# Performance work log

Measured on AMD Instinct MI355X. Metric: run time of the kernel, lower is better.

## Reference

```python
import jax, jax.numpy as jnp
import numpy as np

FSIZE = 128   # fsize
ANUM = 16     # number of agents
CNUM = 2048   # number of cities
BATCH = 64


def setup_inputs() -> dict:
    key = jax.random.key(0)
    ks = jax.random.split(key, 6)
    f = FSIZE
    N = CNUM + 2 * ANUM
    s = 0.02
    return {
        "nfeature": jax.random.normal(ks[0], (BATCH, f, N), jnp.float32),
        # torch Linear weights are [out, in]
        "Wg": jax.random.normal(ks[1], (f, 4 * f), jnp.float32) * s,   # glb_embedding
        "bg": jnp.zeros((f,), jnp.float32),
        "Wc": jax.random.normal(ks[2], (3 * f, 2 * f), jnp.float32) * s,  # city_embedding
        "bc": jnp.zeros((3 * f,), jnp.float32),
        "Wa": jax.random.normal(ks[3], (f, 3 * f), jnp.float32) * s,   # agent_embedding
        "ba": jnp.zeros((f,), jnp.float32),
        "Wp": jax.random.normal(ks[4], (f, f), jnp.float32) * s,       # project_out
        "bp": jnp.zeros((f,), jnp.float32),
        "step": 1,
        "anum": ANUM,
    }


def reference(nfeature, Wg, bg, Wc, bc, Wa, ba, Wp, bp, step, anum):
    nf = jnp.transpose(nfeature, (0, 2, 1))  # [B, N, f]
    B, N, f = nf.shape
    cnum = N - 2 * anum
    city = nf[:, :cnum]                       # [B, cnum, f]
    a_start = nf[:, cnum:cnum + anum]         # [B, anum, f]
    a_end = nf[:, cnum + anum:]               # [B, anum, f]

    # global context via max pooling over segments -> glb_embedding
    glb = jnp.concatenate([nf.max(1), city.max(1), a_start.max(1), a_end.max(1)], axis=1)  # [B, 4f]
    deglb = (glb @ Wg.T + bg)[:, None, :]     # [B, 1, f]

    # mean-pooled global context -> same glb_embedding -> free agent token
    ave = jnp.concatenate([nf.mean(1), city.mean(1), a_start.mean(1), a_end.mean(1)], axis=1)
    free_agent = (ave @ Wg.T + bg)[:, None, :]  # [B, 1, f]

    # city keys/values/logit-keys: x, y, z
    city_feat = jnp.concatenate([jnp.broadcast_to(deglb, (B, cnum, f)), city], axis=2)  # [B, cnum, 2f]
    xyz = city_feat @ Wc.T + bc               # [B, cnum, 3f]
    x, y, z = jnp.split(xyz, 3, axis=2)       # each [B, cnum, f]

    # agent queries
    agent_feat = jnp.concatenate(
        [jnp.broadcast_to(deglb, (B, anum, f)), a_start, a_end], axis=2)  # [B, anum, 3f]
    af = agent_feat @ Wa.T + ba               # [B, anum, f]
    if step > 0:
        af = jnp.concatenate([af, free_agent], axis=1)  # [B, anum+1, f]

    scale = 1.0 / jnp.sqrt(jnp.float32(f))
    ucj = jnp.einsum('baf,bcf->bac', af, x) * scale           # [B, A, cnum]
    new_af = jnp.einsum('bac,bcf->baf', jax.nn.softmax(ucj, axis=2), y)
    new_af = new_af @ Wp.T + bp                                # project_out
    logits = jnp.tanh(jnp.einsum('baf,bcf->bac', new_af, z) * scale) * 10.0  # [B, A, cnum]
    probs = jax.nn.softmax(jnp.transpose(logits, (0, 2, 1)), axis=2)         # [B, cnum, A]
    return probs
```

## Files before the change

kernel.cpp:

```cpp
#include <hip/hip_runtime.h>
#include <math.h>

#define F 128
#define NTOT 2080
#define CN 2048
#define AN 16
#define NA 17
#define CHK 128
#define NCHK 16

__device__ __forceinline__ float wmax(float v){
  #pragma unroll
  for(int m=32;m;m>>=1) v = fmaxf(v, __shfl_xor(v, m, 64));
  return v;
}
__device__ __forceinline__ float wsum(float v){
  #pragma unroll
  for(int m=32;m;m>>=1) v += __shfl_xor(v, m, 64);
  return v;
}

__global__ __launch_bounds__(256) void k0t_transpose(
      const float* __restrict__ Wg, const float* __restrict__ Wc,
      const float* __restrict__ Wp, const float* __restrict__ Wa,
      float* __restrict__ WgT, float* __restrict__ WcT,
      float* __restrict__ WpT, float* __restrict__ WaT){
  __shared__ float tile[32][33];
  const int z = blockIdx.z;
  const float* src; float* dst; int R, C;
  if(z==0){ src=Wg; dst=WgT; R=128; C=512; }
  else if(z==1){ src=Wc; dst=WcT; R=384; C=256; }
  else if(z==2){ src=Wp; dst=WpT; R=128; C=128; }
  else { src=Wa; dst=WaT; R=128; C=384; }
  const int c0 = blockIdx.x*32, r0 = blockIdx.y*32;
  if(c0>=C || r0>=R) return;
  const int tx = threadIdx.x&31, ty = threadIdx.x>>5;
  #pragma unroll
  for(int rr=0;rr<4;rr++)
    tile[ty+rr*8][tx] = src[(size_t)(r0+ty+rr*8)*C + c0 + tx];
  __syncthreads();
  #pragma unroll
  for(int rr=0;rr<4;rr++)
    dst[(size_t)(c0+ty+rr*8)*R + r0 + tx] = tile[tx][ty+rr*8];
}

__global__ __launch_bounds__(128) void k0a_wpy(const float* __restrict__ Wp, const float* __restrict__ Wc,
                                               float* __restrict__ Wpy){
  const int k = blockIdx.x, i = threadIdx.x;
  float acc = 0.f;
  const float* wp = Wp + (size_t)k*F;
  for(int j=0;j<F;j++) acc += wp[j]*Wc[(size_t)(128+j)*256 + 128 + i];
  Wpy[k*F+i] = acc;
}

__global__ __launch_bounds__(128) void k0b_m1(const float* __restrict__ Wc, const float* __restrict__ Wpy,
                                              float* __restrict__ M1){
  const int jc = blockIdx.x, i = threadIdx.x;
  float acc = 0.f;
  for(int k=0;k<F;k++) acc += Wc[(size_t)(256+k)*256 + 128 + jc]*Wpy[k*F+i];
  M1[jc*F+i] = acc;
}

__global__ __launch_bounds__(256) void k1_reduce(const float* __restrict__ nf,
                                                 float* __restrict__ glb, float* __restrict__ ave){
  const int jg = blockIdx.x, b = blockIdx.y;
  const int w = threadIdx.x>>6, lane = threadIdx.x&63;
  const int j = jg*4 + w;
  const float4* row = (const float4*)(nf + (size_t)(b*F + j)*NTOT);
  float cmax=-INFINITY, csum=0.f, smax=-INFINITY, ssum=0.f, emax=-INFINITY, esum=0.f;
  for(int n4 = lane; n4 < 520; n4 += 64){
    float4 v = row[n4];
    float mx = fmaxf(fmaxf(v.x,v.y), fmaxf(v.z,v.w));
    float sm = (v.x+v.y)+(v.z+v.w);
    if(n4 < 512){ cmax=fmaxf(cmax,mx); csum+=sm; }
    else if(n4 < 516){ smax=fmaxf(smax,mx); ssum+=sm; }
    else { emax=fmaxf(emax,mx); esum+=sm; }
  }
  cmax=wmax(cmax); csum=wsum(csum); smax=wmax(smax); ssum=wsum(ssum); emax=wmax(emax); esum=wsum(esum);
  if(lane==0){
    const int gb = b*4*F;
    glb[gb + j]       = fmaxf(cmax, fmaxf(smax,emax));
    glb[gb + F + j]   = cmax;
    glb[gb + 2*F + j] = smax;
    glb[gb + 3*F + j] = emax;
    float tS = csum+ssum+esum;
    ave[gb + j]       = tS / 2080.f;
    ave[gb + F + j]   = csum / 2048.f;
    ave[gb + 2*F + j] = ssum / 16.f;
    ave[gb + 3*F + j] = esum / 16.f;
  }
}

__global__ __launch_bounds__(256) void k2a_prep(
    const float* __restrict__ WgT, const float* __restrict__ bg,
    const float* __restrict__ WcT, const float* __restrict__ Wc, const float* __restrict__ bc,
    const float* __restrict__ WpT, const float* __restrict__ bp,
    const float* __restrict__ Wpy,
    const float* __restrict__ glb, const float* __restrict__ ave,
    float* __restrict__ deglb_g, float* __restrict__ fa_g, float* __restrict__ cx,
    float* __restrict__ czc, float* __restrict__ vz, float* __restrict__ szc){
  const int b = blockIdx.x, tid = threadIdx.x;
  __shared__ float glb_s[512], ave_s[512];
  __shared__ float deglb_s[F], cvec_s[3*F], cpy_s[F];
  for(int i=tid;i<512;i+=256){ glb_s[i]=glb[b*512+i]; ave_s[i]=ave[b*512+i]; }
  __syncthreads();
  {
    const int j = tid&127;
    const float* src = (tid<128)? glb_s : ave_s;
    float a0=0.f,a1=0.f,a2=0.f,a3=0.f;
    for(int k=0;k<512;k+=4){
      a0 += WgT[(size_t)(k+0)*128+j]*src[k+0];
      a1 += WgT[(size_t)(k+1)*128+j]*src[k+1];
      a2 += WgT[(size_t)(k+2)*128+j]*src[k+2];
      a3 += WgT[(size_t)(k+3)*128+j]*src[k+3];
    }
    float d = (a0+a1)+(a2+a3) + bg[j];
    if(tid<128){ deglb_s[j]=d; deglb_g[b*F+j]=d; }
    else fa_g[b*F+j]=d;
  }
  __syncthreads();
  for(int i=tid;i<3*F;i+=256){
    float a0=0.f,a1=0.f,a2=0.f,a3=0.f;
    for(int k=0;k<F;k+=4){
      a0 += WcT[(size_t)(k+0)*384+i]*deglb_s[k+0];
      a1 += WcT[(size_t)(k+1)*384+i]*deglb_s[k+1];
      a2 += WcT[(size_t)(k+2)*384+i]*deglb_s[k+2];
      a3 += WcT[(size_t)(k+3)*384+i]*deglb_s[k+3];
    }
    float v = (a0+a1)+(a2+a3) + bc[i];
    cvec_s[i]=v;
    if(i<F) cx[b*F+i]=v;
  }
  __syncthreads();
  if(tid<128){
    const int j = tid;
    float a0=0.f,a1=0.f,a2=0.f,a3=0.f;
    for(int k=0;k<F;k+=4){
      a0 += WpT[(size_t)(k+0)*128+j]*cvec_s[128+k+0];
      a1 += WpT[(size_t)(k+1)*128+j]*cvec_s[128+k+1];
      a2 += WpT[(size_t)(k+2)*128+j]*cvec_s[128+k+2];
      a3 += WpT[(size_t)(k+3)*128+j]*cvec_s[128+k+3];
    }
    cpy_s[j] = (a0+a1)+(a2+a3) + bp[j];
  } else {
    const int j = tid-128;
    float a0=0.f,a1=0.f,a2=0.f,a3=0.f;
    for(int k=0;k<F;k+=4){
      a0 += Wpy[(size_t)(k+0)*128+j]*cvec_s[256+k+0];
      a1 += Wpy[(size_t)(k+1)*128+j]*cvec_s[256+k+1];
      a2 += Wpy[(size_t)(k+2)*128+j]*cvec_s[256+k+2];
      a3 += Wpy[(size_t)(k+3)*128+j]*cvec_s[256+k+3];
    }
    vz[b*F+j] = (a0+a1)+(a2+a3);
  }
  __syncthreads();
  if(tid<128){
    const int j = tid;
    float a0=0.f,a1=0.f,a2=0.f,a3=0.f;
    for(int k=0;k<F;k+=4){
      a0 += Wc[(size_t)(256+k+0)*256 + 128 + j]*cpy_s[k+0];
      a1 += Wc[(size_t)(256+k+1)*256 + 128 + j]*cpy_s[k+1];
      a2 += Wc[(size_t)(256+k+2)*256 + 128 + j]*cpy_s[k+2];
      a3 += Wc[(size_t)(256+k+3)*256 + 128 + j]*cpy_s[k+3];
    }
    czc[b*F+j] = (a0+a1)+(a2+a3);
  } else if(tid<192){
    const int lane = tid-128;
    float p = cpy_s[lane]*cvec_s[256+lane] + cpy_s[64+lane]*cvec_s[256+64+lane];
    p = wsum(p);
    if(lane==0) szc[b]=p;
  }
}

__global__ __launch_bounds__(256) void k2c_agents(
    const float* __restrict__ nf, const float* __restrict__ WaT, const float* __restrict__ ba,
    const float* __restrict__ Wc,
    const float* __restrict__ deglb_g, const float* __restrict__ fa_g, const float* __restrict__ cx,
    float* __restrict__ afx, float* __restrict__ sx){
  const int a = blockIdx.x, b = blockIdx.y, tid = threadIdx.x;
  __shared__ float src_s[384];
  __shared__ float af_s[F], cx_s[F];
  if(tid<128){ src_s[tid] = deglb_g[b*F+tid]; cx_s[tid]=cx[b*F+tid]; }
  else if(a<16){
    const int j = tid-128;
    src_s[128+j] = nf[(size_t)(b*F+j)*NTOT + CN + a];
    src_s[256+j] = nf[(size_t)(b*F+j)*NTOT + CN + AN + a];
  }
  __syncthreads();
  if(a<16){
    if(tid<128){
      const int j = tid;
      float a0=0.f,a1=0.f,a2=0.f,a3=0.f;
      for(int k=0;k<384;k+=4){
        a0 += WaT[(size_t)(k+0)*128+j]*src_s[k+0];
        a1 += WaT[(size_t)(k+1)*128+j]*src_s[k+1];
        a2 += WaT[(size_t)(k+2)*128+j]*src_s[k+2];
        a3 += WaT[(size_t)(k+3)*128+j]*src_s[k+3];
      }
      af_s[j] = (a0+a1)+(a2+a3) + ba[j];
    }
  } else if(tid<128){
    af_s[tid] = fa_g[b*F+tid];
  }
  __syncthreads();
  if(tid<128){
    const int j = tid;
    float a0=0.f,a1=0.f,a2=0.f,a3=0.f;
    for(int i=0;i<F;i+=4){
      a0 += af_s[i+0]*Wc[(size_t)(i+0)*256 + 128 + j];
      a1 += af_s[i+1]*Wc[(size_t)(i+1)*256 + 128 + j];
      a2 += af_s[i+2]*Wc[(size_t)(i+2)*256 + 128 + j];
      a3 += af_s[i+3]*Wc[(size_t)(i+3)*256 + 128 + j];
    }
    afx[((size_t)b*NA+a)*F + j] = (a0+a1)+(a2+a3);
  } else if(tid<192){
    const int lane = tid-128;
    float p = af_s[lane]*cx_s[lane] + af_s[64+lane]*cx_s[64+lane];
    p = wsum(p);
    if(lane==0) sx[b*NA+a]=p;
  }
}

__global__ __launch_bounds__(256) void k35_flash(const float* __restrict__ nf,
      const float* __restrict__ afx, const float* __restrict__ sx,
      float* __restrict__ pmax, float* __restrict__ psum, float* __restrict__ tpart){
  const int b = blockIdx.y, tid = threadIdx.x;
  const int chunk = blockIdx.x, c0 = chunk*CHK;
  __shared__ float afx_s[NA*F];
  __shared__ float sx_s[NA];
  __shared__ float at_s[NA*CHK];
  __shared__ float4 nf4_s[F*8];
  __shared__ float red_s[4][NA], red2_s[4][NA];
  for(int o=tid;o<NA*F;o+=256) afx_s[o]=afx[(size_t)b*NA*F+o];
  if(tid<NA) sx_s[tid]=sx[b*NA+tid];
  __syncthreads();
  const int kq = tid>>6;
  const int ct = tid&63;
  const int lane = tid&63, w = tid>>6;
  float2 acc[NA];
  #pragma unroll
  for(int a=0;a<NA;a++){ acc[a].x=0.f; acc[a].y=0.f; }
  {
    const float* base = nf + (size_t)b*F*NTOT + (size_t)(kq*32)*NTOT + c0 + 2*ct;
    #pragma unroll 2
    for(int q=0;q<8;q++){
      float2 l0 = *(const float2*)(base + (size_t)(q*4+0)*NTOT);
      float2 l1 = *(const float2*)(base + (size_t)(q*4+1)*NTOT);
      float2 l2 = *(const float2*)(base + (size_t)(q*4+2)*NTOT);
      float2 l3 = *(const float2*)(base + (size_t)(q*4+3)*NTOT);
      #pragma unroll
      for(int a=0;a<NA;a++){
        float4 wv = *(const float4*)&afx_s[a*F + kq*32 + q*4];
        acc[a].x += wv.x*l0.x + wv.y*l1.x + wv.z*l2.x + wv.w*l3.x;
        acc[a].y += wv.x*l0.y + wv.y*l1.y + wv.z*l2.y + wv.w*l3.y;
      }
    }
  }
  for(int k=0;k<4;k++){
    __syncthreads();
    if(kq==k){
      #pragma unroll
      for(int a=0;a<NA;a++){
        float2* p = (float2*)&at_s[a*CHK + 2*ct];
        if(k==0){ *p = acc[a]; }
        else { float2 v = *p; v.x += acc[a].x; v.y += acc[a].y; *p = v; }
      }
    }
  }
  __syncthreads();
  const int cl = tid&127;
  const int hh = tid>>7;
  const int aBeg = hh? 9:0;
  const float scale = 0.088388347648318447f;
  float sc[9];
  #pragma unroll
  for(int a2=0;a2<9;a2++){
    const int a = aBeg+a2;
    if(a<NA){
      sc[a2] = (at_s[a*CHK+cl] + sx_s[a])*scale;
      float mx = wmax(sc[a2]);
      if(lane==0) red_s[w][a]=mx;
    }
  }
  __syncthreads();
  #pragma unroll
  for(int a2=0;a2<9;a2++){
    const int a = aBeg+a2;
    if(a<NA){
      float m = fmaxf(red_s[hh*2][a], red_s[hh*2+1][a]);
      float e = __expf(sc[a2]-m);
      at_s[a*CHK+cl] = e;
      float s = wsum(e);
      if(lane==0) red2_s[w][a]=s;
    }
  }
  __syncthreads();
  if(tid<NA){
    const int base = (tid<9)? 0 : 2;
    pmax[(b*NA+tid)*NCHK + chunk] = fmaxf(red_s[base][tid], red_s[base+1][tid]);
    psum[(b*NA+tid)*NCHK + chunk] = red2_s[base][tid] + red2_s[base+1][tid];
  }
  const int i1 = tid&63;
  const int g2 = (tid>>6)&1;
  const int h  = tid>>7;
  const int A0 = h*8;
  float ta0[9], ta1[9];
  #pragma unroll
  for(int a=0;a<9;a++){ ta0[a]=0.f; ta1[a]=0.f; }
  for(int s4=0;s4<4;s4++){
    const int csl = s4*32, cs = c0 + csl;
    __syncthreads();
    for(int idx=tid; idx<F*8; idx+=256){
      const int ii=idx>>3, g=idx&7;
      nf4_s[ii*8 + (g^(ii&7))] = *(const float4*)(nf + (size_t)(b*F+ii)*NTOT + cs + g*4);
    }
    __syncthreads();
    #pragma unroll
    for(int gg=0; gg<4; gg++){
      const int g = gg*2 + g2;
      float4 v0 = nf4_s[i1*8 + (g^(i1&7))];
      float4 v1 = nf4_s[(i1+64)*8 + (g^(i1&7))];
      #pragma unroll
      for(int a=0;a<9;a++){
        float4 wv = *(const float4*)&at_s[(A0+a)*CHK + csl + g*4];
        ta0[a] += wv.x*v0.x + wv.y*v0.y + wv.z*v0.z + wv.w*v0.w;
        ta1[a] += wv.x*v1.x + wv.y*v1.y + wv.z*v1.z + wv.w*v1.w;
      }
    }
  }
  float* pt = afx_s;
  __syncthreads();
  if(g2==1){
    #pragma unroll
    for(int a=0;a<9;a++){
      pt[(A0+a)*F + i1]      = ta0[a];
      pt[(A0+a)*F + i1 + 64] = ta1[a];
    }
  }
  __syncthreads();
  if(g2==0){
    float* dst = tpart + (size_t)chunk*64*NA*F + (size_t)b*NA*F;
    #pragma unroll
    for(int a=0;a<9;a++){
      if(h==0 || a>0){
        dst[(A0+a)*F + i1]      = ta0[a] + pt[(A0+a)*F + i1];
        dst[(A0+a)*F + i1 + 64] = ta1[a] + pt[(A0+a)*F + i1 + 64];
      }
    }
  }
}

__global__ __launch_bounds__(128) void k5c_final(const float* __restrict__ M1,
      const float* __restrict__ tpart, const float* __restrict__ pmax, const float* __restrict__ psum,
      const float* __restrict__ czc, const float* __restrict__ vz, const float* __restrict__ szc,
      float* __restrict__ afz, float* __restrict__ szv){
  const int a = blockIdx.x, b = blockIdx.y, tid = threadIdx.x;
  __shared__ float tn_s[F];
  const float* pm = pmax + (b*NA+a)*NCHK;
  const float* ps = psum + (b*NA+a)*NCHK;
  float M=-INFINITY;
  #pragma unroll
  for(int k=0;k<NCHK;k++) M = fmaxf(M, pm[k]);
  float w[NCHK]; float rs=0.f;
  #pragma unroll
  for(int k=0;k<NCHK;k++){ w[k]=__expf(pm[k]-M); rs += ps[k]*w[k]; }
  float s = 0.f;
  #pragma unroll
  for(int k=0;k<NCHK;k++) s += tpart[(size_t)k*64*NA*F + ((size_t)b*NA+a)*F + tid]*w[k];
  tn_s[tid] = s / rs;
  __syncthreads();
  float acc = 0.f;
  const float* m = M1 + (size_t)tid*F;
  for(int i=0;i<F;i++) acc += m[i]*tn_s[i];
  afz[((size_t)b*NA+a)*F + tid] = acc + czc[b*F+tid];
  float p = tn_s[tid]*vz[b*F+tid];
  p = wsum(p);
  __shared__ float red[2];
  if((tid&63)==0) red[tid>>6]=p;
  __syncthreads();
  if(tid==0) szv[b*NA+a] = red[0]+red[1] + szc[b];
}

__global__ __launch_bounds__(256) void k6_out(const float* __restrict__ nf, const float* __restrict__ afz,
      const float* __restrict__ szv, const int* __restrict__ step, float* __restrict__ out){
  const int b = blockIdx.y, tid = threadIdx.x;
  const int chunk = blockIdx.x, c0 = chunk*CHK;
  __shared__ float afz_s[NA*F]; __shared__ float sz_s[NA];
  __shared__ float sc_s[NA*CHK];
  for(int o=tid;o<NA*F;o+=256) afz_s[o]=afz[(size_t)b*NA*F+o];
  if(tid<NA) sz_s[tid]=szv[b*NA+tid];
  __syncthreads();
  const int kq = tid>>6, ct = tid&63;
  float2 acc[NA];
  #pragma unroll
  for(int a=0;a<NA;a++){ acc[a].x=0.f; acc[a].y=0.f; }
  {
    const float* base = nf + (size_t)b*F*NTOT + (size_t)(kq*32)*NTOT + c0 + 2*ct;
    #pragma unroll 2
    for(int q=0;q<8;q++){
      float2 l0 = *(const float2*)(base + (size_t)(q*4+0)*NTOT);
      float2 l1 = *(const float2*)(base + (size_t)(q*4+1)*NTOT);
      float2 l2 = *(const float2*)(base + (size_t)(q*4+2)*NTOT);
      float2 l3 = *(const float2*)(base + (size_t)(q*4+3)*NTOT);
      #pragma unroll
      for(int a=0;a<NA;a++){
        float4 wv = *(const float4*)&afz_s[a*F + kq*32 + q*4];
        acc[a].x += wv.x*l0.x + wv.y*l1.x + wv.z*l2.x + wv.w*l3.x;
        acc[a].y += wv.x*l0.y + wv.y*l1.y + wv.z*l2.y + wv.w*l3.y;
      }
    }
  }
  for(int k=0;k<4;k++){
    __syncthreads();
    if(kq==k){
      #pragma unroll
      for(int a=0;a<NA;a++){
        float2* p = (float2*)&sc_s[a*CHK + 2*ct];
        if(k==0){ *p = acc[a]; }
        else { float2 v = *p; v.x += acc[a].x; v.y += acc[a].y; *p = v; }
      }
    }
  }
  __syncthreads();
  if(tid<128){
    const int cl = tid;
    const int A = (step[0] > 0) ? NA : AN;
    const float scale = 0.088388347648318447f;
    float l[NA];
    #pragma unroll
    for(int a=0;a<NA;a++)
      l[a] = tanhf((sc_s[a*CHK+cl] + sz_s[a])*scale)*10.f;
    const bool f17 = (A==NA);
    float m = l[0];
    #pragma unroll
    for(int a=1;a<AN;a++) m = fmaxf(m,l[a]);
    if(f17) m = fmaxf(m,l[16]);
    float ssum=0.f;
    #pragma unroll
    for(int a=0;a<AN;a++){ float e=__expf(l[a]-m); l[a]=e; ssum+=e; }
    float e16=__expf(l[16]-m);
    if(f17){ ssum+=e16; }
    const float inv = 1.f/ssum;
    float* op = out + (size_t)(b*CN + c0 + cl)*A;
    #pragma unroll
    for(int a=0;a<AN;a++) op[a]=l[a]*inv;
    if(f17) op[16]=e16*inv;
  }
}

extern "C" void kernel_launch(void* const* d_in, const int* in_sizes, int n_in,
                              void* d_out, int out_size, void* d_ws, size_t ws_size,
                              hipStream_t stream){
  const float* nf = (const float*)d_in[0];
  const float* Wg = (const float*)d_in[1];
  const float* bg = (const float*)d_in[2];
  const float* Wc = (const float*)d_in[3];
  const float* bc = (const float*)d_in[4];
  const float* Wa = (const float*)d_in[5];
  const float* ba = (const float*)d_in[6];
  const float* Wp = (const float*)d_in[7];
  const float* bp = (const float*)d_in[8];
  const int*  step = (const int*)d_in[9];
  float* out = (float*)d_out;

  float* ws = (float*)d_ws;
  float* glb     = ws;
  float* ave     = glb + 64*512;
  float* afx     = ave + 64*512;
  float* sx      = afx + 64*NA*F;
  float* Wpy     = sx + 64*NA;
  float* M1      = Wpy + F*F;
  float* czc     = M1 + F*F;
  float* vz      = czc + 64*F;
  float* szc     = vz + 64*F;
  float* pmax    = szc + 64;
  float* psum    = pmax + 64*NA*NCHK;
  float* deglb_g = psum + 64*NA*NCHK;
  float* fa_g    = deglb_g + 64*F;
  float* cx      = fa_g + 64*F;
  float* WgT     = cx + 64*F;
  float* WcT     = WgT + 512*F;
  float* WpT     = WcT + 256*384;
  float* WaT     = WpT + F*F;
  float* tpart   = WaT + 384*F;
  float* afz     = tpart + (size_t)NCHK*64*NA*F;
  float* szv     = afz + 64*NA*F;

  k0t_transpose<<<dim3(16,12,4),256,0,stream>>>(Wg,Wc,Wp,Wa, WgT,WcT,WpT,WaT);
  k0a_wpy<<<F,F,0,stream>>>(Wp, Wc, Wpy);
  k0b_m1<<<F,F,0,stream>>>(Wc, Wpy, M1);
  k1_reduce<<<dim3(32,64),256,0,stream>>>(nf, glb, ave);
  k2a_prep<<<64,256,0,stream>>>(WgT,bg, WcT,Wc,bc, WpT,bp, Wpy, glb,ave, deglb_g,fa_g,cx, czc,vz,szc);
  k2c_agents<<<dim3(NA,64),256,0,stream>>>(nf, WaT,ba,Wc, deglb_g,fa_g,cx, afx,sx);
  k35_flash<<<dim3(NCHK,64),256,0,stream>>>(nf, afx, sx, pmax, psum, tpart);
  k5c_final<<<dim3(NA,64),128,0,stream>>>(M1, tpart, pmax, psum, czc, vz, szc, afz, szv);
  k6_out<<<dim3(NCHK,64),256,0,stream>>>(nf, afz, szv, step, out);
}
```

Before: 162.4 us.

## Double chunk size with 512-thread blocks and tree-reduce partial scores

Raises the city chunk to 256 with 512-thread blocks in the flash and output kernels, so there are half as many chunks and partial tpart buffers for the final combine. The serial four-step shared-memory accumulation of the K-split partial scores becomes a two-level tree reduction, and the same is done for the attention-value partials. Each thread now issues scalar loads at two columns instead of float2 loads. This costs more shared memory per block and halves the grid to 512 blocks, which may lower occupancy.

```diff
diff --git a/kernel.cpp b/kernel.cpp
--- a/kernel.cpp
+++ b/kernel.cpp
@@ -6,8 +6,8 @@
 #define CN 2048
 #define AN 16
 #define NA 17
-#define CHK 128
-#define NCHK 16
+#define CHK 256
+#define NCHK 8
 
 __device__ __forceinline__ float wmax(float v){
   #pragma unroll
@@ -221,7 +221,7 @@
   }
 }
 
-__global__ __launch_bounds__(256) void k35_flash(const float* __restrict__ nf,
+__global__ __launch_bounds__(512) void k35_flash(const float* __restrict__ nf,
       const float* __restrict__ afx, const float* __restrict__ sx,
       float* __restrict__ pmax, float* __restrict__ psum, float* __restrict__ tpart){
   const int b = blockIdx.y, tid = threadIdx.x;
@@ -229,55 +229,71 @@
   __shared__ float afx_s[NA*F];
   __shared__ float sx_s[NA];
   __shared__ float at_s[NA*CHK];
+  __shared__ float at2_s[2*NA*CHK];
   __shared__ float4 nf4_s[F*8];
-  __shared__ float red_s[4][NA], red2_s[4][NA];
-  for(int o=tid;o<NA*F;o+=256) afx_s[o]=afx[(size_t)b*NA*F+o];
+  __shared__ float red_s[8][NA], red2_s[8][NA];
+  for(int o=tid;o<NA*F;o+=512) afx_s[o]=afx[(size_t)b*NA*F+o];
   if(tid<NA) sx_s[tid]=sx[b*NA+tid];
   __syncthreads();
-  const int kq = tid>>6;
-  const int ct = tid&63;
-  const int lane = tid&63, w = tid>>6;
-  float2 acc[NA];
-  #pragma unroll
-  for(int a=0;a<NA;a++){ acc[a].x=0.f; acc[a].y=0.f; }
+  const int kq = tid>>7, cl = tid&127;
+  float a0v[NA], a1v[NA];
+  #pragma unroll
+  for(int a=0;a<NA;a++){ a0v[a]=0.f; a1v[a]=0.f; }
   {
-    const float* base = nf + (size_t)b*F*NTOT + (size_t)(kq*32)*NTOT + c0 + 2*ct;
+    const float* base = nf + (size_t)b*F*NTOT + (size_t)(kq*32)*NTOT + c0 + cl;
     #pragma unroll 2
     for(int q=0;q<8;q++){
-      float2 l0 = *(const float2*)(base + (size_t)(q*4+0)*NTOT);
-      float2 l1 = *(const float2*)(base + (size_t)(q*4+1)*NTOT);
-      float2 l2 = *(const float2*)(base + (size_t)(q*4+2)*NTOT);
-      float2 l3 = *(const float2*)(base + (size_t)(q*4+3)*NTOT);
+      const float* r0 = base + (size_t)(q*4)*NTOT;
+      float v0 = r0[0],      u0 = r0[128];
+      float v1 = r0[NTOT],   u1 = r0[NTOT+128];
+      float v2 = r0[2*NTOT], u2 = r0[2*NTOT+128];
+      float v3 = r0[3*NTOT], u3 = r0[3*NTOT+128];
       #pragma unroll
       for(int a=0;a<NA;a++){
         float4 wv = *(const float4*)&afx_s[a*F + kq*32 + q*4];
-        acc[a].x += wv.x*l0.x + wv.y*l1.x + wv.z*l2.x + wv.w*l3.x;
-        acc[a].y += wv.x*l0.y + wv.y*l1.y + wv.z*l2.y + wv.w*l3.y;
+        a0v[a] += wv.x*v0 + wv.y*v1 + wv.z*v2 + wv.w*v3;
+        a1v[a] += wv.x*u0 + wv.y*u1 + wv.z*u2 + wv.w*u3;
       }
     }
   }
-  for(int k=0;k<4;k++){
-    __syncthreads();
-    if(kq==k){
-      #pragma unroll
-      for(int a=0;a<NA;a++){
-        float2* p = (float2*)&at_s[a*CHK + 2*ct];
-        if(k==0){ *p = acc[a]; }
-        else { float2 v = *p; v.x += acc[a].x; v.y += acc[a].y; *p = v; }
-      }
-    }
-  }
-  __syncthreads();
-  const int cl = tid&127;
-  const int hh = tid>>7;
+  if(kq==1){
+    #pragma unroll
+    for(int a=0;a<NA;a++){ at2_s[a*CHK+cl]=a0v[a]; at2_s[a*CHK+cl+128]=a1v[a]; }
+  } else if(kq==3){
+    #pragma unroll
+    for(int a=0;a<NA;a++){ at2_s[NA*CHK+a*CHK+cl]=a0v[a]; at2_s[NA*CHK+a*CHK+cl+128]=a1v[a]; }
+  }
+  __syncthreads();
+  if(kq==0){
+    #pragma unroll
+    for(int a=0;a<NA;a++){ a0v[a]+=at2_s[a*CHK+cl]; a1v[a]+=at2_s[a*CHK+cl+128]; }
+  } else if(kq==2){
+    #pragma unroll
+    for(int a=0;a<NA;a++){
+      at_s[a*CHK+cl]     = a0v[a]+at2_s[NA*CHK+a*CHK+cl];
+      at_s[a*CHK+cl+128] = a1v[a]+at2_s[NA*CHK+a*CHK+cl+128];
+    }
+  }
+  __syncthreads();
+  const float scale = 0.088388347648318447f;
+  if(kq==0){
+    #pragma unroll
+    for(int a=0;a<NA;a++){
+      at_s[a*CHK+cl]     = (a0v[a]+at_s[a*CHK+cl]+sx_s[a])*scale;
+      at_s[a*CHK+cl+128] = (a1v[a]+at_s[a*CHK+cl+128]+sx_s[a])*scale;
+    }
+  }
+  __syncthreads();
+  const int w = tid>>6;
+  const int hh = tid>>8, c = tid&255;
   const int aBeg = hh? 9:0;
-  const float scale = 0.088388347648318447f;
+  const int lane = tid&63;
   float sc[9];
   #pragma unroll
   for(int a2=0;a2<9;a2++){
     const int a = aBeg+a2;
     if(a<NA){
-      sc[a2] = (at_s[a*CHK+cl] + sx_s[a])*scale;
+      sc[a2] = at_s[a*CHK+c];
       float mx = wmax(sc[a2]);
       if(lane==0) red_s[w][a]=mx;
     }
@@ -287,37 +303,39 @@
   for(int a2=0;a2<9;a2++){
     const int a = aBeg+a2;
     if(a<NA){
-      float m = fmaxf(red_s[hh*2][a], red_s[hh*2+1][a]);
+      const int rb = hh*4;
+      float m = fmaxf(fmaxf(red_s[rb][a],red_s[rb+1][a]), fmaxf(red_s[rb+2][a],red_s[rb+3][a]));
       float e = __expf(sc[a2]-m);
-      at_s[a*CHK+cl] = e;
+      at_s[a*CHK+c] = e;
       float s = wsum(e);
       if(lane==0) red2_s[w][a]=s;
     }
   }
   __syncthreads();
   if(tid<NA){
-    const int base = (tid<9)? 0 : 2;
-    pmax[(b*NA+tid)*NCHK + chunk] = fmaxf(red_s[base][tid], red_s[base+1][tid]);
-    psum[(b*NA+tid)*NCHK + chunk] = red2_s[base][tid] + red2_s[base+1][tid];
+    const int rb = (tid<9)? 0 : 4;
+    pmax[(b*NA+tid)*NCHK + chunk] =
+      fmaxf(fmaxf(red_s[rb][tid],red_s[rb+1][tid]), fmaxf(red_s[rb+2][tid],red_s[rb+3][tid]));
+    psum[(b*NA+tid)*NCHK + chunk] =
+      red2_s[rb][tid]+red2_s[rb+1][tid]+red2_s[rb+2][tid]+red2_s[rb+3][tid];
   }
   const int i1 = tid&63;
-  const int g2 = (tid>>6)&1;
-  const int h  = tid>>7;
-  const int A0 = h*8;
+  const int gpar = (tid>>6)&3;
+  const int h = tid>>8, A0 = h*8;
   float ta0[9], ta1[9];
   #pragma unroll
   for(int a=0;a<9;a++){ ta0[a]=0.f; ta1[a]=0.f; }
-  for(int s4=0;s4<4;s4++){
-    const int csl = s4*32, cs = c0 + csl;
+  for(int s8=0;s8<8;s8++){
+    const int csl = s8*32, cs = c0 + csl;
     __syncthreads();
-    for(int idx=tid; idx<F*8; idx+=256){
+    for(int idx=tid; idx<F*8; idx+=512){
       const int ii=idx>>3, g=idx&7;
       nf4_s[ii*8 + (g^(ii&7))] = *(const float4*)(nf + (size_t)(b*F+ii)*NTOT + cs + g*4);
     }
     __syncthreads();
     #pragma unroll
-    for(int gg=0; gg<4; gg++){
-      const int g = gg*2 + g2;
+    for(int gg=0; gg<2; gg++){
+      const int g = gg*4 + gpar;
       float4 v0 = nf4_s[i1*8 + (g^(i1&7))];
       float4 v1 = nf4_s[(i1+64)*8 + (g^(i1&7))];
       #pragma unroll
@@ -328,23 +346,35 @@
       }
     }
   }
-  float* pt = afx_s;
-  __syncthreads();
-  if(g2==1){
+  float* pt0 = at2_s;
+  float* pt1 = at2_s + NA*F;
+  __syncthreads();
+  if(gpar==1){
+    #pragma unroll
+    for(int a=0;a<9;a++){ pt0[(A0+a)*F+i1]=ta0[a]; pt0[(A0+a)*F+i1+64]=ta1[a]; }
+  } else if(gpar==3){
+    #pragma unroll
+    for(int a=0;a<9;a++){ pt1[(A0+a)*F+i1]=ta0[a]; pt1[(A0+a)*F+i1+64]=ta1[a]; }
+  }
+  __syncthreads();
+  if(gpar==2){
     #pragma unroll
     for(int a=0;a<9;a++){
-      pt[(A0+a)*F + i1]      = ta0[a];
-      pt[(A0+a)*F + i1 + 64] = ta1[a];
-    }
-  }
-  __syncthreads();
-  if(g2==0){
+      afx_s[(A0+a)*F+i1]    = ta0[a]+pt1[(A0+a)*F+i1];
+      afx_s[(A0+a)*F+i1+64] = ta1[a]+pt1[(A0+a)*F+i1+64];
+    }
+  } else if(gpar==0){
+    #pragma unroll
+    for(int a=0;a<9;a++){ ta0[a]+=pt0[(A0+a)*F+i1]; ta1[a]+=pt0[(A0+a)*F+i1+64]; }
+  }
+  __syncthreads();
+  if(gpar==0){
     float* dst = tpart + (size_t)chunk*64*NA*F + (size_t)b*NA*F;
     #pragma unroll
     for(int a=0;a<9;a++){
       if(h==0 || a>0){
-        dst[(A0+a)*F + i1]      = ta0[a] + pt[(A0+a)*F + i1];
-        dst[(A0+a)*F + i1 + 64] = ta1[a] + pt[(A0+a)*F + i1 + 64];
+        dst[(A0+a)*F+i1]    = ta0[a]+afx_s[(A0+a)*F+i1];
+        dst[(A0+a)*F+i1+64] = ta1[a]+afx_s[(A0+a)*F+i1+64];
       }
     }
   }
@@ -381,55 +411,73 @@
   if(tid==0) szv[b*NA+a] = red[0]+red[1] + szc[b];
 }
 
-__global__ __launch_bounds__(256) void k6_out(const float* __restrict__ nf, const float* __restrict__ afz,
+__global__ __launch_bounds__(512) void k6_out(const float* __restrict__ nf, const float* __restrict__ afz,
       const float* __restrict__ szv, const int* __restrict__ step, float* __restrict__ out){
   const int b = blockIdx.y, tid = threadIdx.x;
   const int chunk = blockIdx.x, c0 = chunk*CHK;
-  __shared__ float afz_s[NA*F]; __shared__ float sz_s[NA];
-  __shared__ float sc_s[NA*CHK];
-  for(int o=tid;o<NA*F;o+=256) afz_s[o]=afz[(size_t)b*NA*F+o];
+  __shared__ float afz_s[NA*F];
+  __shared__ float sz_s[NA];
+  __shared__ float at_s[NA*CHK];
+  __shared__ float at2_s[2*NA*CHK];
+  for(int o=tid;o<NA*F;o+=512) afz_s[o]=afz[(size_t)b*NA*F+o];
   if(tid<NA) sz_s[tid]=szv[b*NA+tid];
   __syncthreads();
-  const int kq = tid>>6, ct = tid&63;
-  float2 acc[NA];
-  #pragma unroll
-  for(int a=0;a<NA;a++){ acc[a].x=0.f; acc[a].y=0.f; }
+  const int kq = tid>>7, cl = tid&127;
+  float a0v[NA], a1v[NA];
+  #pragma unroll
+  for(int a=0;a<NA;a++){ a0v[a]=0.f; a1v[a]=0.f; }
   {
-    const float* base = nf + (size_t)b*F*NTOT + (size_t)(kq*32)*NTOT + c0 + 2*ct;
+    const float* base = nf + (size_t)b*F*NTOT + (size_t)(kq*32)*NTOT + c0 + cl;
     #pragma unroll 2
     for(int q=0;q<8;q++){
-      float2 l0 = *(const float2*)(base + (size_t)(q*4+0)*NTOT);
-      float2 l1 = *(const float2*)(base + (size_t)(q*4+1)*NTOT);
-      float2 l2 = *(const float2*)(base + (size_t)(q*4+2)*NTOT);
-      float2 l3 = *(const float2*)(base + (size_t)(q*4+3)*NTOT);
+      const float* r0 = base + (size_t)(q*4)*NTOT;
+      float v0 = r0[0],      u0 = r0[128];
+      float v1 = r0[NTOT],   u1 = r0[NTOT+128];
+      float v2 = r0[2*NTOT], u2 = r0[2*NTOT+128];
+      float v3 = r0[3*NTOT], u3 = r0[3*NTOT+128];
       #pragma unroll
       for(int a=0;a<NA;a++){
         float4 wv = *(const float4*)&afz_s[a*F + kq*32 + q*4];
-        acc[a].x += wv.x*l0.x + wv.y*l1.x + wv.z*l2.x + wv.w*l3.x;
-        acc[a].y += wv.x*l0.y + wv.y*l1.y + wv.z*l2.y + wv.w*l3.y;
+        a0v[a] += wv.x*v0 + wv.y*v1 + wv.z*v2 + wv.w*v3;
+        a1v[a] += wv.x*u0 + wv.y*u1 + wv.z*u2 + wv.w*u3;
       }
     }
   }
-  for(int k=0;k<4;k++){
-    __syncthreads();
-    if(kq==k){
-      #pragma unroll
-      for(int a=0;a<NA;a++){
-        float2* p = (float2*)&sc_s[a*CHK + 2*ct];
-        if(k==0){ *p = acc[a]; }
-        else { float2 v = *p; v.x += acc[a].x; v.y += acc[a].y; *p = v; }
-      }
-    }
-  }
-  __syncthreads();
-  if(tid<128){
-    const int cl = tid;
+  if(kq==1){
+    #pragma unroll
+    for(int a=0;a<NA;a++){ at2_s[a*CHK+cl]=a0v[a]; at2_s[a*CHK+cl+128]=a1v[a]; }
+  } else if(kq==3){
+    #pragma unroll
+    for(int a=0;a<NA;a++){ at2_s[NA*CHK+a*CHK+cl]=a0v[a]; at2_s[NA*CHK+a*CHK+cl+128]=a1v[a]; }
+  }
+  __syncthreads();
+  if(kq==0){
+    #pragma unroll
+    for(int a=0;a<NA;a++){ a0v[a]+=at2_s[a*CHK+cl]; a1v[a]+=at2_s[a*CHK+cl+128]; }
+  } else if(kq==2){
+    #pragma unroll
+    for(int a=0;a<NA;a++){
+      at_s[a*CHK+cl]     = a0v[a]+at2_s[NA*CHK+a*CHK+cl];
+      at_s[a*CHK+cl+128] = a1v[a]+at2_s[NA*CHK+a*CHK+cl+128];
+    }
+  }
+  __syncthreads();
+  if(kq==0){
+    #pragma unroll
+    for(int a=0;a<NA;a++){
+      at_s[a*CHK+cl]     += a0v[a];
+      at_s[a*CHK+cl+128] += a1v[a];
+    }
+  }
+  __syncthreads();
+  if(tid<256){
+    const int c = tid;
     const int A = (step[0] > 0) ? NA : AN;
     const float scale = 0.088388347648318447f;
     float l[NA];
     #pragma unroll
     for(int a=0;a<NA;a++)
-      l[a] = tanhf((sc_s[a*CHK+cl] + sz_s[a])*scale)*10.f;
+      l[a] = tanhf((at_s[a*CHK+c] + sz_s[a])*scale)*10.f;
     const bool f17 = (A==NA);
     float m = l[0];
     #pragma unroll
@@ -441,7 +489,7 @@
     float e16=__expf(l[16]-m);
     if(f17){ ssum+=e16; }
     const float inv = 1.f/ssum;
-    float* op = out + (size_t)(b*CN + c0 + cl)*A;
+    float* op = out + (size_t)(b*CN + c0 + c)*A;
     #pragma unroll
     for(int a=0;a<AN;a++) op[a]=l[a]*inv;
     if(f17) op[16]=e16*inv;
@@ -492,7 +540,7 @@
   k1_reduce<<<dim3(32,64),256,0,stream>>>(nf, glb, ave);
   k2a_prep<<<64,256,0,stream>>>(WgT,bg, WcT,Wc,bc, WpT,bp, Wpy, glb,ave, deglb_g,fa_g,cx, czc,vz,szc);
   k2c_agents<<<dim3(NA,64),256,0,stream>>>(nf, WaT,ba,Wc, deglb_g,fa_g,cx, afx,sx);
-  k35_flash<<<dim3(NCHK,64),256,0,stream>>>(nf, afx, sx, pmax, psum, tpart);
+  k35_flash<<<dim3(NCHK,64),512,0,stream>>>(nf, afx, sx, pmax, psum, tpart);
   k5c_final<<<dim3(NA,64),128,0,stream>>>(M1, tpart, pmax, psum, czc, vz, szc, afz, szv);
-  k6_out<<<dim3(NCHK,64),256,0,stream>>>(nf, afz, szv, step, out);
-}
+  k6_out<<<dim3(NCHK,64),512,0,stream>>>(nf, afz, szv, step, out);
+}
```

Measured after the change: 160.1 us. Within noise of the previous version (-1.4%).
